# Kernel optimization log

Measured on AMD Instinct MI355X. Metric: run time of the kernel, lower is better.

The kernel has to match this reference:

```python
import jax, jax.numpy as jnp
import numpy as np

N, F_IN, F_OUT, HEADS = 4096, 128, 64, 4


def setup_inputs() -> dict:
    key = jax.random.key(0)
    k1, k2, k3, k4, k5 = jax.random.split(key, 5)
    X = jax.random.normal(k1, (N, F_IN), dtype=jnp.float32)
    A = jax.random.randint(k2, (N, N), 0, 2, dtype=jnp.int32)
    # zero the diagonal: the torch loop always prepends the self node, so the
    # adjacency must not also contain it (would duplicate the self term).
    A = A * (1 - jnp.eye(N, dtype=jnp.int32))
    # per-head Linear(F_IN, F_OUT) weights/bias and Linear(2*F_OUT, 1, bias=False)
    W = jax.random.normal(k3, (HEADS, F_OUT, F_IN), dtype=jnp.float32) / np.sqrt(F_IN)
    b = jax.random.normal(k4, (HEADS, F_OUT), dtype=jnp.float32) * 0.02
    att = jax.random.normal(k5, (HEADS, 2 * F_OUT), dtype=jnp.float32) / np.sqrt(2 * F_OUT)
    return {"X": X, "A": A, "W": W, "b": b, "att": att}


def reference(X, A, W, b, att):
    # H[h, n, o] = line_h(X)
    H = jnp.einsum('nf,hof->hno', X, W) + b[:, None, :]
    f_out = W.shape[1]
    a_src, a_dst = att[:, :f_out], att[:, f_out:]
    # score e_ij = leaky_relu(a_src.H_i + a_dst.H_j)
    s = jnp.einsum('hno,ho->hn', H, a_src)  # query-side term (xi_bar expanded)
    d = jnp.einsum('hno,ho->hn', H, a_dst)  # neighbor-side term
    e = jax.nn.leaky_relu(s[:, :, None] + d[:, None, :])  # [H, N, N]
    # neighbor set = {self} U {j : A_ij != 0}
    mask = (A > 0) | jnp.eye(A.shape[0], dtype=bool)
    e = jnp.where(mask[None], e, -jnp.inf)
    alpha = jax.nn.softmax(e, axis=-1)  # segment softmax per node row
    # weighted sum per head, then mean over heads (sum / head in the original)
    out = jnp.einsum('hnm,hmo->no', alpha, H) / W.shape[0]
    return out  # [N, F_OUT]
```

## Files before the change

kernel.cpp:

```cpp
#include <hip/hip_runtime.h>
#include <hip/hip_bf16.h>


#define NN 4096
#define FIN 128
#define FOUT 64
#define NH 4

typedef __attribute__((ext_vector_type(8))) short bf16x8;
typedef __attribute__((ext_vector_type(4))) float f32x4;
typedef __attribute__((ext_vector_type(4))) unsigned int u32x4;

__device__ __forceinline__ unsigned short f32_bf16(float f) {
    unsigned u = __builtin_bit_cast(unsigned, f);
    u += 0x7fffu + ((u >> 16) & 1u);
    return (unsigned short)(u >> 16);
}

__global__ __launch_bounds__(256) void pack_bits(
    const int* __restrict__ A, unsigned long long* __restrict__ Abits)
{
    const int row  = blockIdx.x;
    const int lane = threadIdx.x & 63;
    const int wv   = threadIdx.x >> 6;
    const int* arow = A + (size_t)row * NN;
    #pragma unroll 4
    for (int c = 0; c < 16; ++c) {
        const int col = c * 256 + wv * 64 + lane;
        unsigned long long m = __ballot(__builtin_nontemporal_load(&arow[col]) > 0);
        if (lane == 0) Abits[(size_t)row * 64 + c * 4 + wv] = m;
    }
}

__global__ __launch_bounds__(256) void gat_prep(
    const float* __restrict__ X, const float* __restrict__ W,
    const float* __restrict__ b, const float* __restrict__ att,
    unsigned short* __restrict__ HbfT, float* __restrict__ Hrow,
    float* __restrict__ s_out, float* __restrict__ d_out,
    float* __restrict__ es_g, float* __restrict__ es2_g,
    float* __restrict__ ed_g, float* __restrict__ ed2_g)
{
    const int rb = blockIdx.x;
    const int h  = blockIdx.y;
    const int n0 = rb * 32;
    const int t  = threadIdx.x;

    __shared__ float Xl[32][132];
    __shared__ float Wt[128][68];

    for (int g = t; g < 32 * 32; g += 256) {
        int row = g >> 5, c4 = g & 31;
        float4 v = *(const float4*)&X[(size_t)(n0 + row) * FIN + c4 * 4];
        *(float4*)&Xl[row][c4 * 4] = v;
    }
    for (int g = t; g < 64 * 32; g += 256) {
        int o = g >> 5, c4 = g & 31;
        float4 v = *(const float4*)&W[((size_t)h * FOUT + o) * FIN + c4 * 4];
        Wt[c4 * 4 + 0][o] = v.x; Wt[c4 * 4 + 1][o] = v.y;
        Wt[c4 * 4 + 2][o] = v.z; Wt[c4 * 4 + 3][o] = v.w;
    }
    __syncthreads();

    const int rg = t >> 4;
    const int og = t & 15;
    float acc[2][4] = {};

    #pragma unroll 4
    for (int f4 = 0; f4 < 32; ++f4) {
        float xv[2][4], wv[4][4];
        #pragma unroll
        for (int i = 0; i < 2; ++i) {
            float4 tmp = *(const float4*)&Xl[rg * 2 + i][f4 * 4];
            xv[i][0] = tmp.x; xv[i][1] = tmp.y; xv[i][2] = tmp.z; xv[i][3] = tmp.w;
        }
        #pragma unroll
        for (int k = 0; k < 4; ++k) {
            float4 tmp = *(const float4*)&Wt[f4 * 4 + k][og * 4];
            wv[k][0] = tmp.x; wv[k][1] = tmp.y; wv[k][2] = tmp.z; wv[k][3] = tmp.w;
        }
        #pragma unroll
        for (int i = 0; i < 2; ++i)
            #pragma unroll
            for (int k = 0; k < 4; ++k)
                #pragma unroll
                for (int jj = 0; jj < 4; ++jj)
                    acc[i][jj] = fmaf(xv[i][k], wv[k][jj], acc[i][jj]);
    }

    float bb[4], as_[4], ad_[4];
    #pragma unroll
    for (int jj = 0; jj < 4; ++jj) {
        bb[jj]  = b[h * FOUT + og * 4 + jj];
        as_[jj] = att[h * 2 * FOUT + og * 4 + jj];
        ad_[jj] = att[h * 2 * FOUT + FOUT + og * 4 + jj];
    }
    #pragma unroll
    for (int i = 0; i < 2; ++i)
        #pragma unroll
        for (int jj = 0; jj < 4; ++jj)
            acc[i][jj] += bb[jj];

    float sp[2] = {0.f, 0.f}, dp[2] = {0.f, 0.f};
    #pragma unroll
    for (int i = 0; i < 2; ++i)
        #pragma unroll
        for (int jj = 0; jj < 4; ++jj) {
            sp[i] = fmaf(acc[i][jj], as_[jj], sp[i]);
            dp[i] = fmaf(acc[i][jj], ad_[jj], dp[i]);
        }
    #pragma unroll
    for (int off = 1; off < 16; off <<= 1) {
        #pragma unroll
        for (int i = 0; i < 2; ++i) {
            sp[i] += __shfl_xor(sp[i], off);
            dp[i] += __shfl_xor(dp[i], off);
        }
    }
    if (og == 0) {
        #pragma unroll
        for (int i = 0; i < 2; ++i) {
            int nn = n0 + rg * 2 + i;
            s_out[h * NN + nn]  = sp[i];
            d_out[h * NN + nn]  = dp[i];
            es_g [h * NN + nn]  = __expf(sp[i]);
            es2_g[h * NN + nn]  = __expf(0.01f * sp[i]);
            ed_g [h * NN + nn]  = __expf(dp[i]);
            ed2_g[h * NN + nn]  = __expf(0.01f * dp[i]);
        }
    }

    #pragma unroll
    for (int i = 0; i < 2; ++i) {
        float4 v = make_float4(acc[i][0], acc[i][1], acc[i][2], acc[i][3]);
        *(float4*)&Hrow[((size_t)h * NN + n0 + rg * 2 + i) * FOUT + og * 4] = v;
    }
    #pragma unroll
    for (int jj = 0; jj < 4; ++jj) {
        int o = og * 4 + jj;
        ushort2 p;
        p.x = f32_bf16(acc[0][jj]);
        p.y = f32_bf16(acc[1][jj]);
        *(ushort2*)&HbfT[((size_t)h * FOUT + o) * NN + n0 + rg * 2] = p;
    }
}

__global__ __launch_bounds__(512, 8) void gat_main(
    const unsigned* __restrict__ Abits, const unsigned short* __restrict__ HbfT,
    const float* __restrict__ es_g, const float* __restrict__ es2_g,
    const float* __restrict__ ed_g, const float* __restrict__ ed2_g,
    float* __restrict__ Hpart, float* __restrict__ lpartP)
{
    const int id  = blockIdx.x;
    const int grp = id & 31;
    const int h   = grp >> 3;
    const int cg  = grp & 7;
    const int bx  = id >> 5;
    const int n0  = bx * 128;
    const int tid  = threadIdx.x;
    const int w    = tid >> 6;
    const int lane = tid & 63;
    const int r    = lane & 15;
    const int q    = lane >> 4;
    const int qs   = q * 8;

    __shared__ unsigned short Hlds[64][128];
    __shared__ unsigned bits_lds[128 * 5];

    const int n = n0 + w * 16 + r;
    const float es  = es_g [h * NN + n];
    const float es2 = es2_g[h * NN + n];
    const int bits_base = (w * 16 + r) * 5;

    bf16x8 ones;
    #pragma unroll
    for (int i = 0; i < 8; ++i) ones[i] = (short)0x3F80;

    f32x4 acc0 = {0,0,0,0}, acc1 = {0,0,0,0}, acc2 = {0,0,0,0},
          acc3 = {0,0,0,0}, accl = {0,0,0,0};

    for (int ch = 0; ch < 4; ++ch) {
        const int c0 = cg * 512 + ch * 128;
        __syncthreads();

        #pragma unroll
        for (int it = 0; it < 2; ++it) {
            int flat = it * 512 + tid;
            int o    = flat >> 4;
            int c16  = flat & 15;
            int blk  = c16 ^ (o & 15);
            *(bf16x8*)&Hlds[o][blk * 8] =
                *(const bf16x8*)&HbfT[((size_t)h * FOUT + o) * NN + c0 + c16 * 8];
        }
        {
            int row = tid >> 2, wd = tid & 3;
            bits_lds[row * 5 + wd] = Abits[(size_t)(n0 + row) * 128 + (c0 >> 5) + wd];
        }
        __syncthreads();

        const float* edh  = ed_g  + h * NN + c0;
        const float* ed2h = ed2_g + h * NN + c0;

        #pragma unroll
        for (int step = 0; step < 4; ++step) {
            const unsigned bits8 = bits_lds[bits_base + step] >> qs;
            const int mk = step * 32 + qs;

            const float4 e0 = *(const float4*)&edh [mk];
            const float4 e1 = *(const float4*)&edh [mk + 4];
            const float4 g0 = *(const float4*)&ed2h[mk];
            const float4 g1 = *(const float4*)&ed2h[mk + 4];
            const float edv [8] = {e0.x, e0.y, e0.z, e0.w, e1.x, e1.y, e1.z, e1.w};
            const float ed2v[8] = {g0.x, g0.y, g0.z, g0.w, g1.x, g1.y, g1.z, g1.w};

            u32x4 afu;
            #pragma unroll
            for (int p = 0; p < 4; ++p) {
                const int j0 = 2 * p, j1 = 2 * p + 1;
                float wa = (bits8 & (1u << j0))
                         ? fmaxf(es * edv[j0], es2 * ed2v[j0]) : 0.0f;
                float wb = (bits8 & (1u << j1))
                         ? fmaxf(es * edv[j1], es2 * ed2v[j1]) : 0.0f;
                __hip_bfloat162 pk = __float22bfloat162_rn(make_float2(wa, wb));
                unsigned u;
                __builtin_memcpy(&u, &pk, sizeof(u));
                afu[p] = u;
            }
            const bf16x8 af = __builtin_bit_cast(bf16x8, afu);

            const int mb = (step * 4 + q) ^ r;
            const bf16x8 b0 = *(const bf16x8*)&Hlds[r     ][mb * 8];
            const bf16x8 b1 = *(const bf16x8*)&Hlds[r + 16][mb * 8];
            const bf16x8 b2 = *(const bf16x8*)&Hlds[r + 32][mb * 8];
            const bf16x8 b3 = *(const bf16x8*)&Hlds[r + 48][mb * 8];

            acc0 = __builtin_amdgcn_mfma_f32_16x16x32_bf16(af, b0,   acc0, 0, 0, 0);
            acc1 = __builtin_amdgcn_mfma_f32_16x16x32_bf16(af, b1,   acc1, 0, 0, 0);
            acc2 = __builtin_amdgcn_mfma_f32_16x16x32_bf16(af, b2,   acc2, 0, 0, 0);
            acc3 = __builtin_amdgcn_mfma_f32_16x16x32_bf16(af, b3,   acc3, 0, 0, 0);
            accl = __builtin_amdgcn_mfma_f32_16x16x32_bf16(af, ones, accl, 0, 0, 0);
        }
    }

    float* hb = Hpart + ((size_t)(cg * NH + h) * NN + n0 + w * 16) * FOUT;
    #pragma unroll
    for (int reg = 0; reg < 4; ++reg) {
        const int rr = q * 4 + reg;
        hb[rr * FOUT +  0 + r] = acc0[reg];
        hb[rr * FOUT + 16 + r] = acc1[reg];
        hb[rr * FOUT + 32 + r] = acc2[reg];
        hb[rr * FOUT + 48 + r] = acc3[reg];
    }
    if (r == 0) {
        #pragma unroll
        for (int reg = 0; reg < 4; ++reg)
            lpartP[(size_t)(cg * NH + h) * NN + n0 + w * 16 + q * 4 + reg] = accl[reg];
    }
}

__global__ __launch_bounds__(256) void gat_fin(
    const float* __restrict__ Hpart, const float* __restrict__ Hrow,
    const float* __restrict__ lpartP, const float* __restrict__ s_g,
    const float* __restrict__ d_g, float* __restrict__ out)
{
    const int tid = threadIdx.x;
    const int rr  = tid >> 4;
    const int c4  = tid & 15;
    const int n   = blockIdx.x * 16 + rr;
    const int o   = c4 * 4;

    float4 res = make_float4(0.f, 0.f, 0.f, 0.f);
    #pragma unroll
    for (int h = 0; h < NH; ++h) {
        float l = 0.f;
        #pragma unroll
        for (int cg = 0; cg < 8; ++cg)
            l += lpartP[(size_t)(cg * NH + h) * NN + n];
        float tt = s_g[h * NN + n] + d_g[h * NN + n];
        float wd = __expf(fmaxf(tt, 0.01f * tt));
        float inv = 0.25f / (l + wd);

        f32x4 ha = {0.f, 0.f, 0.f, 0.f};
        #pragma unroll
        for (int cg = 0; cg < 8; ++cg) {
            f32x4 hp = __builtin_nontemporal_load(
                (const f32x4*)&Hpart[((size_t)(cg * NH + h) * NN + n) * FOUT + o]);
            ha += hp;
        }
        float4 hr = *(const float4*)&Hrow[((size_t)h * NN + n) * FOUT + o];

        res.x += (ha[0] + wd * hr.x) * inv;
        res.y += (ha[1] + wd * hr.y) * inv;
        res.z += (ha[2] + wd * hr.z) * inv;
        res.w += (ha[3] + wd * hr.w) * inv;
    }
    *(float4*)&out[(size_t)n * FOUT + o] = res;
}

extern "C" void kernel_launch(void* const* d_in, const int* in_sizes, int n_in,
                              void* d_out, int out_size, void* d_ws, size_t ws_size,
                              hipStream_t stream) {
    const float* X   = (const float*)d_in[0];
    const int*   A   = (const int*)  d_in[1];
    const float* W   = (const float*)d_in[2];
    const float* b   = (const float*)d_in[3];
    const float* att = (const float*)d_in[4];
    float* out = (float*)d_out;

    char* ws = (char*)d_ws;
    unsigned short* HbfT = (unsigned short*)ws;
    size_t off = (size_t)NH * FOUT * NN * 2;
    float* s_buf   = (float*)(ws + off);  off += (size_t)NH * NN * 4;
    float* d_buf   = (float*)(ws + off);  off += (size_t)NH * NN * 4;
    float* es_buf  = (float*)(ws + off);  off += (size_t)NH * NN * 4;
    float* es2_buf = (float*)(ws + off);  off += (size_t)NH * NN * 4;
    float* ed_buf  = (float*)(ws + off);  off += (size_t)NH * NN * 4;
    float* ed2_buf = (float*)(ws + off);  off += (size_t)NH * NN * 4;
    unsigned long long* Abits = (unsigned long long*)(ws + off);
    off += (size_t)NN * 64 * 8;
    float* Hrow   = (float*)(ws + off);
    off += (size_t)NH * NN * FOUT * 4;
    float* Hpart  = (float*)(ws + off);
    off += (size_t)8 * NH * NN * FOUT * 4;
    float* lpartP = (float*)(ws + off);
    off += (size_t)8 * NH * NN * 4;

    pack_bits<<<NN, 256, 0, stream>>>(A, Abits);
    gat_prep<<<dim3(128, 4), 256, 0, stream>>>(X, W, b, att, HbfT, Hrow,
                                               s_buf, d_buf,
                                               es_buf, es2_buf, ed_buf, ed2_buf);
    gat_main<<<1024, 512, 0, stream>>>((const unsigned*)Abits, HbfT,
                                       es_buf, es2_buf, ed_buf, ed2_buf,
                                       Hpart, lpartP);
    gat_fin<<<256, 256, 0, stream>>>(Hpart, Hrow, lpartP, s_buf, d_buf, out);
}
```

Measured before the change: 168.5 us.

## Restructure GAT main kernel: full-K per block, double-buffered LDS, in-block reduction

Each block of gat_main now covers 32 rows of one head across all 4096 columns instead of splitting columns into 8 groups. The 8 waves split the K dimension four ways and combine partial sums through shared memory. Loads of the HbfT tile and the adjacency bits are double-buffered in registers and LDS to overlap global loads with MFMA work. Normalisation and the self term move into the main kernel, so the 8-way Hpart/lpart partial buffers and their traffic go away, and the final kernel only sums the four heads. The cost is fewer blocks (512), more LDS per block, and an extra reduction step.

```diff
diff --git a/kernel.cpp b/kernel.cpp
--- a/kernel.cpp
+++ b/kernel.cpp
@@ -144,32 +144,49 @@
     }
 }
 
-__global__ __launch_bounds__(512, 8) void gat_main(
+__global__ __launch_bounds__(512, 4) void gat_main(
     const unsigned* __restrict__ Abits, const unsigned short* __restrict__ HbfT,
+    const float* __restrict__ s_g, const float* __restrict__ d_g,
     const float* __restrict__ es_g, const float* __restrict__ es2_g,
     const float* __restrict__ ed_g, const float* __restrict__ ed2_g,
-    float* __restrict__ Hpart, float* __restrict__ lpartP)
+    const float* __restrict__ Hrow, float* __restrict__ outH)
 {
-    const int id  = blockIdx.x;
-    const int grp = id & 31;
-    const int h   = grp >> 3;
-    const int cg  = grp & 7;
-    const int bx  = id >> 5;
-    const int n0  = bx * 128;
+    const int id   = blockIdx.x;
+    const int h    = id & 3;
+    const int tile = id >> 2;
+    const int n0   = tile * 32;
     const int tid  = threadIdx.x;
     const int w    = tid >> 6;
     const int lane = tid & 63;
     const int r    = lane & 15;
     const int q    = lane >> 4;
     const int qs   = q * 8;
-
-    __shared__ unsigned short Hlds[64][128];
-    __shared__ unsigned bits_lds[128 * 5];
-
-    const int n = n0 + w * 16 + r;
-    const float es  = es_g [h * NN + n];
-    const float es2 = es2_g[h * NN + n];
-    const int bits_base = (w * 16 + r) * 5;
+    const int rg   = w & 1;
+    const int kg   = w >> 1;
+
+    __shared__ __align__(16) unsigned short Hlds[2][64][128];
+    __shared__ unsigned bits_lds[2][32 * 5];
+    __shared__ float red[6][16][68];
+    __shared__ float redl[6][16];
+
+    const int nrow = n0 + rg * 16 + r;
+    const float es  = es_g [h * NN + nrow];
+    const float es2 = es2_g[h * NN + nrow];
+
+    const int mb       = (kg * 4 + q) ^ r;
+    const int bits_idx = (rg * 16 + r) * 5 + kg;
+
+    const int so = tid >> 4;
+    const int sc = tid & 15;
+    const unsigned short* srcA = HbfT + ((size_t)(h * FOUT) + so)      * NN + sc * 8;
+    const unsigned short* srcB = HbfT + ((size_t)(h * FOUT) + so + 32) * NN + sc * 8;
+    const int offA = so * 128        + (sc ^ (so & 15)) * 8;
+    const int offB = (so + 32) * 128 + (sc ^ (so & 15)) * 8;
+    const int brow = tid >> 2, bwd = tid & 3;
+    const unsigned* srcBits = Abits + (size_t)(n0 + brow) * 128 + bwd;
+
+    const float* edh  = ed_g  + h * NN + kg * 32 + qs;
+    const float* ed2h = ed2_g + h * NN + kg * 32 + qs;
 
     bf16x8 ones;
     #pragma unroll
@@ -178,122 +195,133 @@
     f32x4 acc0 = {0,0,0,0}, acc1 = {0,0,0,0}, acc2 = {0,0,0,0},
           acc3 = {0,0,0,0}, accl = {0,0,0,0};
 
-    for (int ch = 0; ch < 4; ++ch) {
-        const int c0 = cg * 512 + ch * 128;
+    bf16x8 stA, stB;
+    unsigned stBits = 0;
+
+    stA = *(const bf16x8*)&srcA[0];
+    stB = *(const bf16x8*)&srcB[0];
+    {
+        unsigned short* hw = &Hlds[0][0][0];
+        *(bf16x8*)(hw + offA) = stA;
+        *(bf16x8*)(hw + offB) = stB;
+        if (tid < 128) bits_lds[0][brow * 5 + bwd] = srcBits[0];
+    }
+    __syncthreads();
+
+    for (int ch = 0; ch < 32; ++ch) {
+        const int buf = ch & 1;
+        const unsigned short* hb = buf ? &Hlds[1][0][0] : &Hlds[0][0][0];
+        const unsigned*       bl = buf ? bits_lds[1]    : bits_lds[0];
+
+        if (ch < 31) {
+            stA = *(const bf16x8*)&srcA[(ch + 1) * 128];
+            stB = *(const bf16x8*)&srcB[(ch + 1) * 128];
+            if (tid < 128) stBits = srcBits[(ch + 1) * 4];
+        }
+
+        const unsigned bits8 = bl[bits_idx] >> qs;
+        const int cb = ch * 128;
+        const float4 e0 = *(const float4*)&edh [cb];
+        const float4 e1 = *(const float4*)&edh [cb + 4];
+        const float4 g0 = *(const float4*)&ed2h[cb];
+        const float4 g1 = *(const float4*)&ed2h[cb + 4];
+        const float edv [8] = {e0.x, e0.y, e0.z, e0.w, e1.x, e1.y, e1.z, e1.w};
+        const float ed2v[8] = {g0.x, g0.y, g0.z, g0.w, g1.x, g1.y, g1.z, g1.w};
+
+        u32x4 afu;
+        #pragma unroll
+        for (int p = 0; p < 4; ++p) {
+            const int j0 = 2 * p, j1 = 2 * p + 1;
+            float wa = (bits8 & (1u << j0))
+                     ? fmaxf(es * edv[j0], es2 * ed2v[j0]) : 0.0f;
+            float wb = (bits8 & (1u << j1))
+                     ? fmaxf(es * edv[j1], es2 * ed2v[j1]) : 0.0f;
+            __hip_bfloat162 pk = __float22bfloat162_rn(make_float2(wa, wb));
+            unsigned u;
+            __builtin_memcpy(&u, &pk, sizeof(u));
+            afu[p] = u;
+        }
+        const bf16x8 af = __builtin_bit_cast(bf16x8, afu);
+
+        const bf16x8 b0 = *(const bf16x8*)&hb[(r     ) * 128 + mb * 8];
+        const bf16x8 b1 = *(const bf16x8*)&hb[(r + 16) * 128 + mb * 8];
+        const bf16x8 b2 = *(const bf16x8*)&hb[(r + 32) * 128 + mb * 8];
+        const bf16x8 b3 = *(const bf16x8*)&hb[(r + 48) * 128 + mb * 8];
+
+        acc0 = __builtin_amdgcn_mfma_f32_16x16x32_bf16(af, b0,   acc0, 0, 0, 0);
+        acc1 = __builtin_amdgcn_mfma_f32_16x16x32_bf16(af, b1,   acc1, 0, 0, 0);
+        acc2 = __builtin_amdgcn_mfma_f32_16x16x32_bf16(af, b2,   acc2, 0, 0, 0);
+        acc3 = __builtin_amdgcn_mfma_f32_16x16x32_bf16(af, b3,   acc3, 0, 0, 0);
+        accl = __builtin_amdgcn_mfma_f32_16x16x32_bf16(af, ones, accl, 0, 0, 0);
+
+        if (ch < 31) {
+            unsigned short* hw = buf ? &Hlds[0][0][0] : &Hlds[1][0][0];
+            *(bf16x8*)(hw + offA) = stA;
+            *(bf16x8*)(hw + offB) = stB;
+            if (tid < 128) (buf ? bits_lds[0] : bits_lds[1])[brow * 5 + bwd] = stBits;
+        }
         __syncthreads();
-
-        #pragma unroll
-        for (int it = 0; it < 2; ++it) {
-            int flat = it * 512 + tid;
-            int o    = flat >> 4;
-            int c16  = flat & 15;
-            int blk  = c16 ^ (o & 15);
-            *(bf16x8*)&Hlds[o][blk * 8] =
-                *(const bf16x8*)&HbfT[((size_t)h * FOUT + o) * NN + c0 + c16 * 8];
-        }
-        {
-            int row = tid >> 2, wd = tid & 3;
-            bits_lds[row * 5 + wd] = Abits[(size_t)(n0 + row) * 128 + (c0 >> 5) + wd];
-        }
-        __syncthreads();
-
-        const float* edh  = ed_g  + h * NN + c0;
-        const float* ed2h = ed2_g + h * NN + c0;
-
-        #pragma unroll
-        for (int step = 0; step < 4; ++step) {
-            const unsigned bits8 = bits_lds[bits_base + step] >> qs;
-            const int mk = step * 32 + qs;
-
-            const float4 e0 = *(const float4*)&edh [mk];
-            const float4 e1 = *(const float4*)&edh [mk + 4];
-            const float4 g0 = *(const float4*)&ed2h[mk];
-            const float4 g1 = *(const float4*)&ed2h[mk + 4];
-            const float edv [8] = {e0.x, e0.y, e0.z, e0.w, e1.x, e1.y, e1.z, e1.w};
-            const float ed2v[8] = {g0.x, g0.y, g0.z, g0.w, g1.x, g1.y, g1.z, g1.w};
-
-            u32x4 afu;
+    }
+
+    if (kg > 0) {
+        const int widx = (kg - 1) * 2 + rg;
+        #pragma unroll
+        for (int reg = 0; reg < 4; ++reg) {
+            const int rr = q * 4 + reg;
+            red[widx][rr][ 0 + r] = acc0[reg];
+            red[widx][rr][16 + r] = acc1[reg];
+            red[widx][rr][32 + r] = acc2[reg];
+            red[widx][rr][48 + r] = acc3[reg];
+        }
+        if (r == 0) {
             #pragma unroll
-            for (int p = 0; p < 4; ++p) {
-                const int j0 = 2 * p, j1 = 2 * p + 1;
-                float wa = (bits8 & (1u << j0))
-                         ? fmaxf(es * edv[j0], es2 * ed2v[j0]) : 0.0f;
-                float wb = (bits8 & (1u << j1))
-                         ? fmaxf(es * edv[j1], es2 * ed2v[j1]) : 0.0f;
-                __hip_bfloat162 pk = __float22bfloat162_rn(make_float2(wa, wb));
-                unsigned u;
-                __builtin_memcpy(&u, &pk, sizeof(u));
-                afu[p] = u;
+            for (int reg = 0; reg < 4; ++reg)
+                redl[widx][q * 4 + reg] = accl[reg];
+        }
+    }
+    __syncthreads();
+    if (kg == 0) {
+        #pragma unroll
+        for (int kk = 0; kk < 3; ++kk) {
+            const int widx = kk * 2 + rg;
+            #pragma unroll
+            for (int reg = 0; reg < 4; ++reg) {
+                const int rr = q * 4 + reg;
+                acc0[reg] += red[widx][rr][ 0 + r];
+                acc1[reg] += red[widx][rr][16 + r];
+                acc2[reg] += red[widx][rr][32 + r];
+                acc3[reg] += red[widx][rr][48 + r];
+                accl[reg] += redl[widx][rr];
             }
-            const bf16x8 af = __builtin_bit_cast(bf16x8, afu);
-
-            const int mb = (step * 4 + q) ^ r;
-            const bf16x8 b0 = *(const bf16x8*)&Hlds[r     ][mb * 8];
-            const bf16x8 b1 = *(const bf16x8*)&Hlds[r + 16][mb * 8];
-            const bf16x8 b2 = *(const bf16x8*)&Hlds[r + 32][mb * 8];
-            const bf16x8 b3 = *(const bf16x8*)&Hlds[r + 48][mb * 8];
-
-            acc0 = __builtin_amdgcn_mfma_f32_16x16x32_bf16(af, b0,   acc0, 0, 0, 0);
-            acc1 = __builtin_amdgcn_mfma_f32_16x16x32_bf16(af, b1,   acc1, 0, 0, 0);
-            acc2 = __builtin_amdgcn_mfma_f32_16x16x32_bf16(af, b2,   acc2, 0, 0, 0);
-            acc3 = __builtin_amdgcn_mfma_f32_16x16x32_bf16(af, b3,   acc3, 0, 0, 0);
-            accl = __builtin_amdgcn_mfma_f32_16x16x32_bf16(af, ones, accl, 0, 0, 0);
-        }
-    }
-
-    float* hb = Hpart + ((size_t)(cg * NH + h) * NN + n0 + w * 16) * FOUT;
-    #pragma unroll
-    for (int reg = 0; reg < 4; ++reg) {
-        const int rr = q * 4 + reg;
-        hb[rr * FOUT +  0 + r] = acc0[reg];
-        hb[rr * FOUT + 16 + r] = acc1[reg];
-        hb[rr * FOUT + 32 + r] = acc2[reg];
-        hb[rr * FOUT + 48 + r] = acc3[reg];
-    }
-    if (r == 0) {
-        #pragma unroll
-        for (int reg = 0; reg < 4; ++reg)
-            lpartP[(size_t)(cg * NH + h) * NN + n0 + w * 16 + q * 4 + reg] = accl[reg];
+        }
+        #pragma unroll
+        for (int reg = 0; reg < 4; ++reg) {
+            const int rr  = q * 4 + reg;
+            const int nn2 = n0 + rg * 16 + rr;
+            const float tt = s_g[h * NN + nn2] + d_g[h * NN + nn2];
+            const float wd = __expf(fmaxf(tt, 0.01f * tt));
+            const float inv = 0.25f / (accl[reg] + wd);
+            const float* hr = &Hrow[((size_t)h * NN + nn2) * FOUT];
+            float*       ob = &outH[((size_t)h * NN + nn2) * FOUT];
+            ob[ 0 + r] = (acc0[reg] + wd * hr[ 0 + r]) * inv;
+            ob[16 + r] = (acc1[reg] + wd * hr[16 + r]) * inv;
+            ob[32 + r] = (acc2[reg] + wd * hr[32 + r]) * inv;
+            ob[48 + r] = (acc3[reg] + wd * hr[48 + r]) * inv;
+        }
     }
 }
 
 __global__ __launch_bounds__(256) void gat_fin(
-    const float* __restrict__ Hpart, const float* __restrict__ Hrow,
-    const float* __restrict__ lpartP, const float* __restrict__ s_g,
-    const float* __restrict__ d_g, float* __restrict__ out)
+    const float* __restrict__ outH, float* __restrict__ out)
 {
-    const int tid = threadIdx.x;
-    const int rr  = tid >> 4;
-    const int c4  = tid & 15;
-    const int n   = blockIdx.x * 16 + rr;
-    const int o   = c4 * 4;
-
-    float4 res = make_float4(0.f, 0.f, 0.f, 0.f);
-    #pragma unroll
-    for (int h = 0; h < NH; ++h) {
-        float l = 0.f;
-        #pragma unroll
-        for (int cg = 0; cg < 8; ++cg)
-            l += lpartP[(size_t)(cg * NH + h) * NN + n];
-        float tt = s_g[h * NN + n] + d_g[h * NN + n];
-        float wd = __expf(fmaxf(tt, 0.01f * tt));
-        float inv = 0.25f / (l + wd);
-
-        f32x4 ha = {0.f, 0.f, 0.f, 0.f};
-        #pragma unroll
-        for (int cg = 0; cg < 8; ++cg) {
-            f32x4 hp = __builtin_nontemporal_load(
-                (const f32x4*)&Hpart[((size_t)(cg * NH + h) * NN + n) * FOUT + o]);
-            ha += hp;
-        }
-        float4 hr = *(const float4*)&Hrow[((size_t)h * NN + n) * FOUT + o];
-
-        res.x += (ha[0] + wd * hr.x) * inv;
-        res.y += (ha[1] + wd * hr.y) * inv;
-        res.z += (ha[2] + wd * hr.z) * inv;
-        res.w += (ha[3] + wd * hr.w) * inv;
-    }
-    *(float4*)&out[(size_t)n * FOUT + o] = res;
+    const int i = blockIdx.x * 256 + threadIdx.x;
+    const f32x4* p = (const f32x4*)outH;
+    f32x4 v0 = __builtin_nontemporal_load(p + i);
+    f32x4 v1 = __builtin_nontemporal_load(p + i +  65536);
+    f32x4 v2 = __builtin_nontemporal_load(p + i + 131072);
+    f32x4 v3 = __builtin_nontemporal_load(p + i + 196608);
+    f32x4 s = (v0 + v1) + (v2 + v3);
+    *((f32x4*)out + i) = s;
 }
 
 extern "C" void kernel_launch(void* const* d_in, const int* in_sizes, int n_in,
@@ -319,17 +347,16 @@
     off += (size_t)NN * 64 * 8;
     float* Hrow   = (float*)(ws + off);
     off += (size_t)NH * NN * FOUT * 4;
-    float* Hpart  = (float*)(ws + off);
-    off += (size_t)8 * NH * NN * FOUT * 4;
-    float* lpartP = (float*)(ws + off);
-    off += (size_t)8 * NH * NN * 4;
+    float* outH   = (float*)(ws + off);
+    off += (size_t)NH * NN * FOUT * 4;
 
     pack_bits<<<NN, 256, 0, stream>>>(A, Abits);
     gat_prep<<<dim3(128, 4), 256, 0, stream>>>(X, W, b, att, HbfT, Hrow,
                                                s_buf, d_buf,
                                                es_buf, es2_buf, ed_buf, ed2_buf);
-    gat_main<<<1024, 512, 0, stream>>>((const unsigned*)Abits, HbfT,
-                                       es_buf, es2_buf, ed_buf, ed2_buf,
-                                       Hpart, lpartP);
-    gat_fin<<<256, 256, 0, stream>>>(Hpart, Hrow, lpartP, s_buf, d_buf, out);
-}
+    gat_main<<<512, 512, 0, stream>>>((const unsigned*)Abits, HbfT,
+                                      s_buf, d_buf,
+                                      es_buf, es2_buf, ed_buf, ed2_buf,
+                                      Hrow, outH);
+    gat_fin<<<256, 256, 0, stream>>>(outH, out);
+}
```

Result: no change. 166.7 us (-1.1%).
